# Kernel tuning notes

Hardware: AMD Instinct MI355X
Metric: run time of the kernel (lower is better)

## Reference

```python
import jax, jax.numpy as jnp
import numpy as np

DIM = 768
HQ = 8
HKV = 2
HD = 64
B = 1
S = 4096


def setup_inputs() -> dict:
    key = jax.random.key(0)
    ks = jax.random.split(key, 9)
    s = 0.02
    return {
        "x": jax.random.normal(ks[0], (B, S, DIM), jnp.float32),
        "Wq": jax.random.normal(ks[1], (DIM, HQ * HD), jnp.float32) * s,
        "bq": jax.random.normal(ks[2], (HQ * HD,), jnp.float32) * s,
        "Wk": jax.random.normal(ks[3], (DIM, HKV * HD), jnp.float32) * s,
        "bk": jax.random.normal(ks[4], (HKV * HD,), jnp.float32) * s,
        "Wv": jax.random.normal(ks[5], (DIM, HKV * HD), jnp.float32) * s,
        "bv": jax.random.normal(ks[6], (HKV * HD,), jnp.float32) * s,
        "Wo": jax.random.normal(ks[7], (HQ * HD, DIM), jnp.float32) * s,
        "bo": jax.random.normal(ks[8], (DIM,), jnp.float32) * s,
    }


def reference(x, Wq, bq, Wk, bk, Wv, bv, Wo, bo):
    bsz, q_len, _ = x.shape
    n_rep = HQ // HKV
    # projections
    q = (x @ Wq + bq).reshape(bsz, q_len, HQ, HD).transpose(0, 2, 1, 3)   # [b,hq,s,d]
    k = (x @ Wk + bk).reshape(bsz, q_len, HKV, HD).transpose(0, 2, 1, 3)  # [b,hkv,s,d]
    v = (x @ Wv + bv).reshape(bsz, q_len, HKV, HD).transpose(0, 2, 1, 3)
    # repeat_kv: expand kv heads to match query heads
    k = jnp.broadcast_to(k[:, :, None], (bsz, HKV, n_rep, q_len, HD)).reshape(bsz, HQ, q_len, HD)
    v = jnp.broadcast_to(v[:, :, None], (bsz, HKV, n_rep, q_len, HD)).reshape(bsz, HQ, q_len, HD)
    # full materialized attention (no mask in the original)
    att = jnp.einsum("bhqd,bhkd->bhqk", q, k) / jnp.sqrt(jnp.float32(HD))
    att = jax.nn.softmax(att.astype(jnp.float32), axis=-1).astype(q.dtype)  # [b,hq,s,s]
    out = jnp.einsum("bhqk,bhkd->bhqd", att, v)
    out = out.transpose(0, 2, 1, 3).reshape(bsz, q_len, HQ * HD)
    out = out @ Wo + bo
    return (out, att)
```

## Files before the change

kernel.cpp:

```cpp
#include <hip/hip_runtime.h>
#include <hip/hip_bf16.h>


#define DIM   768
#define Sc    4096

typedef __bf16 bfrag __attribute__((ext_vector_type(8)));
typedef float  facc  __attribute__((ext_vector_type(4)));

#define MFMA_BF16(a,b,c) __builtin_amdgcn_mfma_f32_16x16x32_bf16((a),(b),(c),0,0,0)

__global__ __launch_bounds__(256) void prep_kernel(
    const float* __restrict__ x,  const float* __restrict__ Wq,
    const float* __restrict__ Wk, const float* __restrict__ Wv,
    const float* __restrict__ Wo,
    __bf16* __restrict__ xb, __bf16* __restrict__ WqkvT, __bf16* __restrict__ WobT)
{
  int i = blockIdx.x * 256 + threadIdx.x;
  const int NX = Sc * DIM;
  const int NW = DIM * DIM;
  if (i < NX) { xb[i] = (__bf16)x[i]; return; }
  i -= NX;
  if (i < NW) {
    int n = i / DIM, c = i - n * DIM;
    float v;
    if (n < 512)      v = Wq[c * 512 + n];
    else if (n < 640) v = Wk[c * 128 + (n - 512)];
    else              v = Wv[c * 128 + (n - 640)];
    WqkvT[i] = (__bf16)v;
    return;
  }
  i -= NW;
  {
    int n = i / 512, k = i - n * 512;
    WobT[i] = (__bf16)Wo[k * DIM + n];
  }
}

template<int MODE>
__global__ __launch_bounds__(256) void gemm_kernel(
    const __bf16* __restrict__ A, const __bf16* __restrict__ BT, int Kd,
    const float* __restrict__ b0, const float* __restrict__ b1, const float* __restrict__ b2,
    __bf16* __restrict__ Qb, __bf16* __restrict__ Kb, __bf16* __restrict__ VTb,
    float* __restrict__ Cout)
{
  const int tid  = threadIdx.x;
  const int w    = tid >> 6;
  const int lane = tid & 63;
  const int i16  = lane & 15;
  const int quad = lane >> 4;
  const int n0   = blockIdx.x * 64;
  const int m0   = blockIdx.y * 128;

  __shared__ __attribute__((aligned(16))) __bf16 Al[128 * 72];
  __shared__ __attribute__((aligned(16))) __bf16 Bl[64 * 72];

  facc acc[2][4];
#pragma unroll
  for (int mt = 0; mt < 2; ++mt)
#pragma unroll
    for (int nt = 0; nt < 4; ++nt)
      acc[mt][nt] = (facc){0.f, 0.f, 0.f, 0.f};

  const int nkt = Kd >> 6;
  for (int kt = 0; kt < nkt; ++kt) {
#pragma unroll
    for (int it = 0; it < 4; ++it) {
      int idx = tid + it * 256;
      int r = idx >> 3, ch = idx & 7;
      *(uint4*)&Al[r * 72 + ch * 8] =
          *(const uint4*)(A + (size_t)(m0 + r) * Kd + (kt * 64 + ch * 8));
    }
#pragma unroll
    for (int it = 0; it < 2; ++it) {
      int idx = tid + it * 256;
      int r = idx >> 3, ch = idx & 7;
      *(uint4*)&Bl[r * 72 + ch * 8] =
          *(const uint4*)(BT + (size_t)(n0 + r) * Kd + (kt * 64 + ch * 8));
    }
    __syncthreads();
#pragma unroll
    for (int ks = 0; ks < 2; ++ks) {
      bfrag a0 = *(const bfrag*)&Al[(w * 32 + i16) * 72 + ks * 32 + quad * 8];
      bfrag a1 = *(const bfrag*)&Al[(w * 32 + 16 + i16) * 72 + ks * 32 + quad * 8];
#pragma unroll
      for (int nt = 0; nt < 4; ++nt) {
        bfrag b = *(const bfrag*)&Bl[(nt * 16 + i16) * 72 + ks * 32 + quad * 8];
        acc[0][nt] = MFMA_BF16(a0, b, acc[0][nt]);
        acc[1][nt] = MFMA_BF16(a1, b, acc[1][nt]);
      }
    }
    __syncthreads();
  }

#pragma unroll
  for (int mt = 0; mt < 2; ++mt)
#pragma unroll
    for (int nt = 0; nt < 4; ++nt) {
      const int n = n0 + nt * 16 + i16;
      const int rbase = m0 + w * 32 + mt * 16 + quad * 4;
      if (MODE == 0) {
        float bias;
        if (n < 512)      bias = b0[n];
        else if (n < 640) bias = b1[n - 512];
        else              bias = b2[n - 640];
#pragma unroll
        for (int reg = 0; reg < 4; ++reg) {
          float v = acc[mt][nt][reg] + bias;
          int row = rbase + reg;
          if (n < 512) {
            int hh = n >> 6, d = n & 63;
            Qb[((size_t)hh * Sc + row) * 64 + d] = (__bf16)(v * 0.125f);
          } else if (n < 640) {
            int hh = (n - 512) >> 6, d = n & 63;
            Kb[((size_t)hh * Sc + row) * 64 + d] = (__bf16)v;
          } else {
            int hh = (n - 640) >> 6, d = n & 63;
            VTb[(size_t)hh * 64 * Sc + (size_t)d * Sc + row] = (__bf16)v;
          }
        }
      } else {
        float bias = b0[n];
#pragma unroll
        for (int reg = 0; reg < 4; ++reg)
          Cout[(size_t)(rbase + reg) * DIM + n] = acc[mt][nt][reg] + bias;
      }
    }
}

__global__ __launch_bounds__(256) void attn_kernel(
    const __bf16* __restrict__ Qb, const __bf16* __restrict__ Kb,
    const __bf16* __restrict__ VTb,
    float* __restrict__ att, __bf16* __restrict__ OAb)
{
  const int tid  = threadIdx.x;
  const int w    = tid >> 6;
  const int lane = tid & 63;
  const int i16  = lane & 15;
  const int quad = lane >> 4;
  const int h    = blockIdx.y;
  const int kvh  = h >> 2;
  const int q0   = blockIdx.x * 128;

  __shared__ __attribute__((aligned(16))) __bf16 Kl[64 * 72];
  __shared__ __attribute__((aligned(16))) __bf16 Vl[64 * 72];
  __shared__ __attribute__((aligned(16))) __bf16 Pl[128 * 72];

  bfrag qf[2][2];
#pragma unroll
  for (int mt = 0; mt < 2; ++mt)
#pragma unroll
    for (int ks = 0; ks < 2; ++ks)
      qf[mt][ks] = *(const bfrag*)(Qb +
          ((size_t)h * Sc + q0 + w * 32 + mt * 16 + i16) * 64 + ks * 32 + quad * 8);

  float mrun[2][4], lrun[2][4];
#pragma unroll
  for (int mt = 0; mt < 2; ++mt)
#pragma unroll
    for (int r = 0; r < 4; ++r) { mrun[mt][r] = -1e30f; lrun[mt][r] = 0.f; }

  const __bf16* Kbase = Kb  + (size_t)kvh * Sc * 64;
  const __bf16* Vbase = VTb + (size_t)kvh * 64 * Sc;

  for (int kt = 0; kt < 64; ++kt) {
#pragma unroll
    for (int it = 0; it < 2; ++it) {
      int idx = tid + it * 256; int r = idx >> 3, ch = idx & 7;
      *(uint4*)&Kl[r * 72 + ch * 8] =
          *(const uint4*)(Kbase + (size_t)(kt * 64 + r) * 64 + ch * 8);
    }
    __syncthreads();
    facc s[2][4];
#pragma unroll
    for (int mt = 0; mt < 2; ++mt)
#pragma unroll
      for (int nt = 0; nt < 4; ++nt)
        s[mt][nt] = (facc){0.f, 0.f, 0.f, 0.f};
#pragma unroll
    for (int ks = 0; ks < 2; ++ks)
#pragma unroll
      for (int mt = 0; mt < 2; ++mt) {
        bfrag a = qf[mt][ks];
#pragma unroll
        for (int nt = 0; nt < 4; ++nt) {
          bfrag b = *(const bfrag*)&Kl[(nt * 16 + i16) * 72 + ks * 32 + quad * 8];
          s[mt][nt] = MFMA_BF16(a, b, s[mt][nt]);
        }
      }
#pragma unroll
    for (int mt = 0; mt < 2; ++mt)
#pragma unroll
      for (int r = 0; r < 4; ++r) {
        float tm = fmaxf(fmaxf(s[mt][0][r], s[mt][1][r]), fmaxf(s[mt][2][r], s[mt][3][r]));
        tm = fmaxf(tm, __shfl_xor(tm, 1));
        tm = fmaxf(tm, __shfl_xor(tm, 2));
        tm = fmaxf(tm, __shfl_xor(tm, 4));
        tm = fmaxf(tm, __shfl_xor(tm, 8));
        float mnew = fmaxf(mrun[mt][r], tm);
        float ts = __expf(s[mt][0][r] - mnew) + __expf(s[mt][1][r] - mnew)
                 + __expf(s[mt][2][r] - mnew) + __expf(s[mt][3][r] - mnew);
        ts += __shfl_xor(ts, 1);
        ts += __shfl_xor(ts, 2);
        ts += __shfl_xor(ts, 4);
        ts += __shfl_xor(ts, 8);
        lrun[mt][r] = lrun[mt][r] * __expf(mrun[mt][r] - mnew) + ts;
        mrun[mt][r] = mnew;
      }
    __syncthreads();
  }

  float linv[2][4];
#pragma unroll
  for (int mt = 0; mt < 2; ++mt)
#pragma unroll
    for (int r = 0; r < 4; ++r) linv[mt][r] = 1.f / lrun[mt][r];

  facc oacc[2][4];
#pragma unroll
  for (int mt = 0; mt < 2; ++mt)
#pragma unroll
    for (int nt = 0; nt < 4; ++nt)
      oacc[mt][nt] = (facc){0.f, 0.f, 0.f, 0.f};

  float* attb = att + (size_t)h * Sc * Sc;

  for (int kt = 0; kt < 64; ++kt) {
#pragma unroll
    for (int it = 0; it < 2; ++it) {
      int idx = tid + it * 256; int r = idx >> 3, ch = idx & 7;
      *(uint4*)&Kl[r * 72 + ch * 8] =
          *(const uint4*)(Kbase + (size_t)(kt * 64 + r) * 64 + ch * 8);
    }
#pragma unroll
    for (int it = 0; it < 2; ++it) {
      int idx = tid + it * 256; int r = idx >> 3, ch = idx & 7;
      *(uint4*)&Vl[r * 72 + ch * 8] =
          *(const uint4*)(Vbase + (size_t)r * Sc + kt * 64 + ch * 8);
    }
    __syncthreads();
    facc s[2][4];
#pragma unroll
    for (int mt = 0; mt < 2; ++mt)
#pragma unroll
      for (int nt = 0; nt < 4; ++nt)
        s[mt][nt] = (facc){0.f, 0.f, 0.f, 0.f};
#pragma unroll
    for (int ks = 0; ks < 2; ++ks)
#pragma unroll
      for (int mt = 0; mt < 2; ++mt) {
        bfrag a = qf[mt][ks];
#pragma unroll
        for (int nt = 0; nt < 4; ++nt) {
          bfrag b = *(const bfrag*)&Kl[(nt * 16 + i16) * 72 + ks * 32 + quad * 8];
          s[mt][nt] = MFMA_BF16(a, b, s[mt][nt]);
        }
      }
#pragma unroll
    for (int mt = 0; mt < 2; ++mt)
#pragma unroll
      for (int nt = 0; nt < 4; ++nt)
#pragma unroll
        for (int r = 0; r < 4; ++r) {
          float p = __expf(s[mt][nt][r] - mrun[mt][r]) * linv[mt][r];
          int row = q0 + w * 32 + mt * 16 + quad * 4 + r;
          attb[(size_t)row * Sc + kt * 64 + nt * 16 + i16] = p;
          Pl[(w * 32 + mt * 16 + quad * 4 + r) * 72 + nt * 16 + i16] = (__bf16)p;
        }
#pragma unroll
    for (int ks = 0; ks < 2; ++ks)
#pragma unroll
      for (int mt = 0; mt < 2; ++mt) {
        bfrag pa = *(const bfrag*)&Pl[(w * 32 + mt * 16 + i16) * 72 + ks * 32 + quad * 8];
#pragma unroll
        for (int nt = 0; nt < 4; ++nt) {
          bfrag bvv = *(const bfrag*)&Vl[(nt * 16 + i16) * 72 + ks * 32 + quad * 8];
          oacc[mt][nt] = MFMA_BF16(pa, bvv, oacc[mt][nt]);
        }
      }
    __syncthreads();
  }

#pragma unroll
  for (int mt = 0; mt < 2; ++mt)
#pragma unroll
    for (int nt = 0; nt < 4; ++nt)
#pragma unroll
      for (int r = 0; r < 4; ++r) {
        int row = q0 + w * 32 + mt * 16 + quad * 4 + r;
        OAb[(size_t)row * 512 + h * 64 + nt * 16 + i16] = (__bf16)oacc[mt][nt][r];
      }
}

extern "C" void kernel_launch(void* const* d_in, const int* in_sizes, int n_in,
                              void* d_out, int out_size, void* d_ws, size_t ws_size,
                              hipStream_t stream) {
  const float* x  = (const float*)d_in[0];
  const float* Wq = (const float*)d_in[1];
  const float* bq = (const float*)d_in[2];
  const float* Wk = (const float*)d_in[3];
  const float* bk = (const float*)d_in[4];
  const float* Wv = (const float*)d_in[5];
  const float* bv = (const float*)d_in[6];
  const float* Wo = (const float*)d_in[7];
  const float* bo = (const float*)d_in[8];

  float* out = (float*)d_out;
  float* att = out + (size_t)Sc * DIM;

  char* ws = (char*)d_ws;
  size_t off = 0;
  __bf16* xb    = (__bf16*)(ws + off); off += (size_t)Sc * DIM * 2;
  __bf16* WqkvT = (__bf16*)(ws + off); off += (size_t)DIM * DIM * 2;
  __bf16* WobT  = (__bf16*)(ws + off); off += (size_t)DIM * 512 * 2;
  __bf16* Qb    = (__bf16*)(ws + off); off += (size_t)8 * Sc * 64 * 2;
  __bf16* Kb    = (__bf16*)(ws + off); off += (size_t)2 * Sc * 64 * 2;
  __bf16* VTb   = (__bf16*)(ws + off); off += (size_t)2 * 64 * Sc * 2;
  __bf16* OAb   = (__bf16*)(ws + off); off += (size_t)Sc * 512 * 2;

  prep_kernel<<<16128, 256, 0, stream>>>(x, Wq, Wk, Wv, Wo, xb, WqkvT, WobT);
  gemm_kernel<0><<<dim3(12, 32), 256, 0, stream>>>(xb, WqkvT, 768, bq, bk, bv,
                                                   Qb, Kb, VTb, nullptr);
  attn_kernel<<<dim3(32, 8), 256, 0, stream>>>(Qb, Kb, VTb, att, OAb);
  gemm_kernel<1><<<dim3(12, 32), 256, 0, stream>>>(OAb, WobT, 512, bo, nullptr, nullptr,
                                                   nullptr, nullptr, nullptr, out);
}
```

Measured before the change: 929.2 us.

## Split attention keys across waves with 16-query blocks and coalesced att stores

The attention kernel now processes 16 query rows per block and splits the 4096 keys across the four waves. Each wave keeps its own softmax statistics, and these are merged through shared memory before the second pass. Probabilities are staged in LDS so the large fp32 attention matrix is written with coalesced 16-byte stores, and K/V are read directly from global memory rather than through shared tiles. The GEMMs use 64-row tiles with twice as many blocks, trading per-block reuse for more parallelism. The attention grid grows to 2048 blocks with a launch-bounds occupancy hint, at the cost of more redundant K/V loads from L2.

```diff
diff --git a/kernel.cpp b/kernel.cpp
--- a/kernel.cpp
+++ b/kernel.cpp
@@ -50,22 +50,19 @@
   const int i16  = lane & 15;
   const int quad = lane >> 4;
   const int n0   = blockIdx.x * 64;
-  const int m0   = blockIdx.y * 128;
-
-  __shared__ __attribute__((aligned(16))) __bf16 Al[128 * 72];
+  const int m0   = blockIdx.y * 64;
+
+  __shared__ __attribute__((aligned(16))) __bf16 Al[64 * 72];
   __shared__ __attribute__((aligned(16))) __bf16 Bl[64 * 72];
 
-  facc acc[2][4];
-#pragma unroll
-  for (int mt = 0; mt < 2; ++mt)
-#pragma unroll
-    for (int nt = 0; nt < 4; ++nt)
-      acc[mt][nt] = (facc){0.f, 0.f, 0.f, 0.f};
+  facc acc[4];
+#pragma unroll
+  for (int nt = 0; nt < 4; ++nt) acc[nt] = (facc){0.f, 0.f, 0.f, 0.f};
 
   const int nkt = Kd >> 6;
   for (int kt = 0; kt < nkt; ++kt) {
 #pragma unroll
-    for (int it = 0; it < 4; ++it) {
+    for (int it = 0; it < 2; ++it) {
       int idx = tid + it * 256;
       int r = idx >> 3, ch = idx & 7;
       *(uint4*)&Al[r * 72 + ch * 8] =
@@ -81,54 +78,53 @@
     __syncthreads();
 #pragma unroll
     for (int ks = 0; ks < 2; ++ks) {
-      bfrag a0 = *(const bfrag*)&Al[(w * 32 + i16) * 72 + ks * 32 + quad * 8];
-      bfrag a1 = *(const bfrag*)&Al[(w * 32 + 16 + i16) * 72 + ks * 32 + quad * 8];
+      bfrag a = *(const bfrag*)&Al[(w * 16 + i16) * 72 + ks * 32 + quad * 8];
 #pragma unroll
       for (int nt = 0; nt < 4; ++nt) {
         bfrag b = *(const bfrag*)&Bl[(nt * 16 + i16) * 72 + ks * 32 + quad * 8];
-        acc[0][nt] = MFMA_BF16(a0, b, acc[0][nt]);
-        acc[1][nt] = MFMA_BF16(a1, b, acc[1][nt]);
+        acc[nt] = MFMA_BF16(a, b, acc[nt]);
       }
     }
     __syncthreads();
   }
 
 #pragma unroll
-  for (int mt = 0; mt < 2; ++mt)
-#pragma unroll
-    for (int nt = 0; nt < 4; ++nt) {
-      const int n = n0 + nt * 16 + i16;
-      const int rbase = m0 + w * 32 + mt * 16 + quad * 4;
-      if (MODE == 0) {
-        float bias;
-        if (n < 512)      bias = b0[n];
-        else if (n < 640) bias = b1[n - 512];
-        else              bias = b2[n - 640];
-#pragma unroll
-        for (int reg = 0; reg < 4; ++reg) {
-          float v = acc[mt][nt][reg] + bias;
-          int row = rbase + reg;
-          if (n < 512) {
-            int hh = n >> 6, d = n & 63;
-            Qb[((size_t)hh * Sc + row) * 64 + d] = (__bf16)(v * 0.125f);
-          } else if (n < 640) {
-            int hh = (n - 512) >> 6, d = n & 63;
-            Kb[((size_t)hh * Sc + row) * 64 + d] = (__bf16)v;
-          } else {
-            int hh = (n - 640) >> 6, d = n & 63;
-            VTb[(size_t)hh * 64 * Sc + (size_t)d * Sc + row] = (__bf16)v;
-          }
+  for (int nt = 0; nt < 4; ++nt) {
+    const int n = n0 + nt * 16 + i16;
+    const int rbase = m0 + w * 16 + quad * 4;
+    if (MODE == 0) {
+      float bias;
+      if (n < 512)      bias = b0[n];
+      else if (n < 640) bias = b1[n - 512];
+      else              bias = b2[n - 640];
+#pragma unroll
+      for (int reg = 0; reg < 4; ++reg) {
+        float v = acc[nt][reg] + bias;
+        int row = rbase + reg;
+        if (n < 512) {
+          int hh = n >> 6, d = n & 63;
+          Qb[((size_t)hh * Sc + row) * 64 + d] = (__bf16)(v * 0.125f);
+        } else if (n < 640) {
+          int hh = (n - 512) >> 6, d = n & 63;
+          Kb[((size_t)hh * Sc + row) * 64 + d] = (__bf16)v;
+        } else {
+          int hh = (n - 640) >> 6, d = n & 63;
+          VTb[(size_t)hh * 64 * Sc + (size_t)d * Sc + row] = (__bf16)v;
         }
-      } else {
-        float bias = b0[n];
-#pragma unroll
-        for (int reg = 0; reg < 4; ++reg)
-          Cout[(size_t)(rbase + reg) * DIM + n] = acc[mt][nt][reg] + bias;
-      }
-    }
+      }
+    } else {
+      float bias = b0[n];
+#pragma unroll
+      for (int reg = 0; reg < 4; ++reg)
+        Cout[(size_t)(rbase + reg) * DIM + n] = acc[nt][reg] + bias;
+    }
+  }
 }
 
-__global__ __launch_bounds__(256) void attn_kernel(
+#define PFSTRIDE 68
+#define PFWAVE   (16 * PFSTRIDE + 4)
+
+__global__ __launch_bounds__(256, 6) void attn_kernel(
     const __bf16* __restrict__ Qb, const __bf16* __restrict__ Kb,
     const __bf16* __restrict__ VTb,
     float* __restrict__ att, __bf16* __restrict__ OAb)
@@ -140,156 +136,138 @@
   const int quad = lane >> 4;
   const int h    = blockIdx.y;
   const int kvh  = h >> 2;
-  const int q0   = blockIdx.x * 128;
-
-  __shared__ __attribute__((aligned(16))) __bf16 Kl[64 * 72];
-  __shared__ __attribute__((aligned(16))) __bf16 Vl[64 * 72];
-  __shared__ __attribute__((aligned(16))) __bf16 Pl[128 * 72];
-
-  bfrag qf[2][2];
-#pragma unroll
-  for (int mt = 0; mt < 2; ++mt)
-#pragma unroll
-    for (int ks = 0; ks < 2; ++ks)
-      qf[mt][ks] = *(const bfrag*)(Qb +
-          ((size_t)h * Sc + q0 + w * 32 + mt * 16 + i16) * 64 + ks * 32 + quad * 8);
-
-  float mrun[2][4], lrun[2][4];
-#pragma unroll
-  for (int mt = 0; mt < 2; ++mt)
-#pragma unroll
-    for (int r = 0; r < 4; ++r) { mrun[mt][r] = -1e30f; lrun[mt][r] = 0.f; }
+  const int q0   = blockIdx.x * 16;
+
+  __shared__ __attribute__((aligned(16))) float Pf[4 * PFWAVE];
+  __shared__ float SM[4][16], SL[4][16];
 
   const __bf16* Kbase = Kb  + (size_t)kvh * Sc * 64;
   const __bf16* Vbase = VTb + (size_t)kvh * 64 * Sc;
 
-  for (int kt = 0; kt < 64; ++kt) {
-#pragma unroll
-    for (int it = 0; it < 2; ++it) {
-      int idx = tid + it * 256; int r = idx >> 3, ch = idx & 7;
-      *(uint4*)&Kl[r * 72 + ch * 8] =
-          *(const uint4*)(Kbase + (size_t)(kt * 64 + r) * 64 + ch * 8);
-    }
-    __syncthreads();
-    facc s[2][4];
-#pragma unroll
-    for (int mt = 0; mt < 2; ++mt)
-#pragma unroll
-      for (int nt = 0; nt < 4; ++nt)
-        s[mt][nt] = (facc){0.f, 0.f, 0.f, 0.f};
+  bfrag qf[2];
+#pragma unroll
+  for (int ks = 0; ks < 2; ++ks)
+    qf[ks] = *(const bfrag*)(Qb + ((size_t)h * Sc + q0 + i16) * 64 + ks * 32 + quad * 8);
+
+  float mrun[4], lrun[4];
+#pragma unroll
+  for (int r = 0; r < 4; ++r) { mrun[r] = -1e30f; lrun[r] = 0.f; }
+
+  const int key0 = w * 1024;
+
+  for (int kt = 0; kt < 16; ++kt) {
+    const int kb0 = key0 + kt * 64;
+    facc s[4];
+#pragma unroll
+    for (int nt = 0; nt < 4; ++nt) s[nt] = (facc){0.f, 0.f, 0.f, 0.f};
 #pragma unroll
     for (int ks = 0; ks < 2; ++ks)
 #pragma unroll
-      for (int mt = 0; mt < 2; ++mt) {
-        bfrag a = qf[mt][ks];
-#pragma unroll
-        for (int nt = 0; nt < 4; ++nt) {
-          bfrag b = *(const bfrag*)&Kl[(nt * 16 + i16) * 72 + ks * 32 + quad * 8];
-          s[mt][nt] = MFMA_BF16(a, b, s[mt][nt]);
-        }
-      }
-#pragma unroll
-    for (int mt = 0; mt < 2; ++mt)
-#pragma unroll
-      for (int r = 0; r < 4; ++r) {
-        float tm = fmaxf(fmaxf(s[mt][0][r], s[mt][1][r]), fmaxf(s[mt][2][r], s[mt][3][r]));
-        tm = fmaxf(tm, __shfl_xor(tm, 1));
-        tm = fmaxf(tm, __shfl_xor(tm, 2));
-        tm = fmaxf(tm, __shfl_xor(tm, 4));
-        tm = fmaxf(tm, __shfl_xor(tm, 8));
-        float mnew = fmaxf(mrun[mt][r], tm);
-        float ts = __expf(s[mt][0][r] - mnew) + __expf(s[mt][1][r] - mnew)
-                 + __expf(s[mt][2][r] - mnew) + __expf(s[mt][3][r] - mnew);
-        ts += __shfl_xor(ts, 1);
-        ts += __shfl_xor(ts, 2);
-        ts += __shfl_xor(ts, 4);
-        ts += __shfl_xor(ts, 8);
-        lrun[mt][r] = lrun[mt][r] * __expf(mrun[mt][r] - mnew) + ts;
-        mrun[mt][r] = mnew;
-      }
-    __syncthreads();
-  }
-
-  float linv[2][4];
-#pragma unroll
-  for (int mt = 0; mt < 2; ++mt)
-#pragma unroll
-    for (int r = 0; r < 4; ++r) linv[mt][r] = 1.f / lrun[mt][r];
-
-  facc oacc[2][4];
-#pragma unroll
-  for (int mt = 0; mt < 2; ++mt)
+      for (int nt = 0; nt < 4; ++nt) {
+        bfrag kf = *(const bfrag*)(Kbase + (size_t)(kb0 + nt * 16 + i16) * 64 + ks * 32 + quad * 8);
+        s[nt] = MFMA_BF16(qf[ks], kf, s[nt]);
+      }
+#pragma unroll
+    for (int r = 0; r < 4; ++r) {
+      float tm = fmaxf(fmaxf(s[0][r], s[1][r]), fmaxf(s[2][r], s[3][r]));
+      tm = fmaxf(tm, __shfl_xor(tm, 1));
+      tm = fmaxf(tm, __shfl_xor(tm, 2));
+      tm = fmaxf(tm, __shfl_xor(tm, 4));
+      tm = fmaxf(tm, __shfl_xor(tm, 8));
+      float mnew = fmaxf(mrun[r], tm);
+      float ts = __expf(s[0][r] - mnew) + __expf(s[1][r] - mnew)
+               + __expf(s[2][r] - mnew) + __expf(s[3][r] - mnew);
+      ts += __shfl_xor(ts, 1);
+      ts += __shfl_xor(ts, 2);
+      ts += __shfl_xor(ts, 4);
+      ts += __shfl_xor(ts, 8);
+      lrun[r] = lrun[r] * __expf(mrun[r] - mnew) + ts;
+      mrun[r] = mnew;
+    }
+  }
+
+  if (i16 == 0) {
+#pragma unroll
+    for (int r = 0; r < 4; ++r) { SM[w][quad * 4 + r] = mrun[r]; SL[w][quad * 4 + r] = lrun[r]; }
+  }
+  __syncthreads();
+  float mglob[4], linv[4];
+#pragma unroll
+  for (int r = 0; r < 4; ++r) {
+    const int rr = quad * 4 + r;
+    float m0v = SM[0][rr], m1v = SM[1][rr], m2v = SM[2][rr], m3v = SM[3][rr];
+    float mg = fmaxf(fmaxf(m0v, m1v), fmaxf(m2v, m3v));
+    float lg = SL[0][rr] * __expf(m0v - mg) + SL[1][rr] * __expf(m1v - mg)
+             + SL[2][rr] * __expf(m2v - mg) + SL[3][rr] * __expf(m3v - mg);
+    mglob[r] = mg;
+    linv[r]  = 1.f / lg;
+  }
+
+  facc oacc[4];
+#pragma unroll
+  for (int nt = 0; nt < 4; ++nt) oacc[nt] = (facc){0.f, 0.f, 0.f, 0.f};
+
+  float* attb = att + (size_t)h * Sc * Sc;
+  float* Pw   = Pf + w * PFWAVE;
+
+  for (int kt = 0; kt < 16; ++kt) {
+    const int kb0 = key0 + kt * 64;
+    facc s[4];
+#pragma unroll
+    for (int nt = 0; nt < 4; ++nt) s[nt] = (facc){0.f, 0.f, 0.f, 0.f};
+#pragma unroll
+    for (int ks = 0; ks < 2; ++ks)
+#pragma unroll
+      for (int nt = 0; nt < 4; ++nt) {
+        bfrag kf = *(const bfrag*)(Kbase + (size_t)(kb0 + nt * 16 + i16) * 64 + ks * 32 + quad * 8);
+        s[nt] = MFMA_BF16(qf[ks], kf, s[nt]);
+      }
 #pragma unroll
     for (int nt = 0; nt < 4; ++nt)
-      oacc[mt][nt] = (facc){0.f, 0.f, 0.f, 0.f};
-
-  float* attb = att + (size_t)h * Sc * Sc;
-
-  for (int kt = 0; kt < 64; ++kt) {
-#pragma unroll
-    for (int it = 0; it < 2; ++it) {
-      int idx = tid + it * 256; int r = idx >> 3, ch = idx & 7;
-      *(uint4*)&Kl[r * 72 + ch * 8] =
-          *(const uint4*)(Kbase + (size_t)(kt * 64 + r) * 64 + ch * 8);
-    }
-#pragma unroll
-    for (int it = 0; it < 2; ++it) {
-      int idx = tid + it * 256; int r = idx >> 3, ch = idx & 7;
-      *(uint4*)&Vl[r * 72 + ch * 8] =
-          *(const uint4*)(Vbase + (size_t)r * Sc + kt * 64 + ch * 8);
-    }
-    __syncthreads();
-    facc s[2][4];
-#pragma unroll
-    for (int mt = 0; mt < 2; ++mt)
-#pragma unroll
-      for (int nt = 0; nt < 4; ++nt)
-        s[mt][nt] = (facc){0.f, 0.f, 0.f, 0.f};
+#pragma unroll
+      for (int r = 0; r < 4; ++r)
+        Pw[(quad * 4 + r) * PFSTRIDE + nt * 16 + i16] =
+            __expf(s[nt][r] - mglob[r]) * linv[r];
+    bfrag pa[2];
+#pragma unroll
+    for (int ks = 0; ks < 2; ++ks) {
+      facc p0 = *(const facc*)&Pw[i16 * PFSTRIDE + ks * 32 + quad * 8];
+      facc p1 = *(const facc*)&Pw[i16 * PFSTRIDE + ks * 32 + quad * 8 + 4];
+      bfrag t;
+      t[0] = (__bf16)p0[0]; t[1] = (__bf16)p0[1]; t[2] = (__bf16)p0[2]; t[3] = (__bf16)p0[3];
+      t[4] = (__bf16)p1[0]; t[5] = (__bf16)p1[1]; t[6] = (__bf16)p1[2]; t[7] = (__bf16)p1[3];
+      pa[ks] = t;
+    }
 #pragma unroll
     for (int ks = 0; ks < 2; ++ks)
 #pragma unroll
-      for (int mt = 0; mt < 2; ++mt) {
-        bfrag a = qf[mt][ks];
-#pragma unroll
-        for (int nt = 0; nt < 4; ++nt) {
-          bfrag b = *(const bfrag*)&Kl[(nt * 16 + i16) * 72 + ks * 32 + quad * 8];
-          s[mt][nt] = MFMA_BF16(a, b, s[mt][nt]);
-        }
-      }
-#pragma unroll
-    for (int mt = 0; mt < 2; ++mt)
-#pragma unroll
-      for (int nt = 0; nt < 4; ++nt)
-#pragma unroll
-        for (int r = 0; r < 4; ++r) {
-          float p = __expf(s[mt][nt][r] - mrun[mt][r]) * linv[mt][r];
-          int row = q0 + w * 32 + mt * 16 + quad * 4 + r;
-          attb[(size_t)row * Sc + kt * 64 + nt * 16 + i16] = p;
-          Pl[(w * 32 + mt * 16 + quad * 4 + r) * 72 + nt * 16 + i16] = (__bf16)p;
-        }
-#pragma unroll
-    for (int ks = 0; ks < 2; ++ks)
-#pragma unroll
-      for (int mt = 0; mt < 2; ++mt) {
-        bfrag pa = *(const bfrag*)&Pl[(w * 32 + mt * 16 + i16) * 72 + ks * 32 + quad * 8];
-#pragma unroll
-        for (int nt = 0; nt < 4; ++nt) {
-          bfrag bvv = *(const bfrag*)&Vl[(nt * 16 + i16) * 72 + ks * 32 + quad * 8];
-          oacc[mt][nt] = MFMA_BF16(pa, bvv, oacc[mt][nt]);
-        }
-      }
-    __syncthreads();
-  }
-
-#pragma unroll
-  for (int mt = 0; mt < 2; ++mt)
-#pragma unroll
-    for (int nt = 0; nt < 4; ++nt)
-#pragma unroll
-      for (int r = 0; r < 4; ++r) {
-        int row = q0 + w * 32 + mt * 16 + quad * 4 + r;
-        OAb[(size_t)row * 512 + h * 64 + nt * 16 + i16] = (__bf16)oacc[mt][nt][r];
-      }
+      for (int nt = 0; nt < 4; ++nt) {
+        bfrag vf = *(const bfrag*)(Vbase + (size_t)(nt * 16 + i16) * Sc + kb0 + ks * 32 + quad * 8);
+        oacc[nt] = MFMA_BF16(pa[ks], vf, oacc[nt]);
+      }
+#pragma unroll
+    for (int it = 0; it < 4; ++it) {
+      int flat = it * 64 + lane;
+      int row = flat >> 4, c4 = flat & 15;
+      facc v = *(const facc*)&Pw[row * PFSTRIDE + c4 * 4];
+      *(facc*)&attb[(size_t)(q0 + row) * Sc + kb0 + c4 * 4] = v;
+    }
+  }
+
+#pragma unroll
+  for (int nt = 0; nt < 4; ++nt)
+#pragma unroll
+    for (int r = 0; r < 4; ++r)
+      Pw[(quad * 4 + r) * PFSTRIDE + nt * 16 + i16] = oacc[nt][r];
+  __syncthreads();
+#pragma unroll
+  for (int it = 0; it < 4; ++it) {
+    int e = it * 256 + tid;
+    int row = e >> 6, d = e & 63;
+    float sum = Pf[0 * PFWAVE + row * PFSTRIDE + d] + Pf[1 * PFWAVE + row * PFSTRIDE + d]
+              + Pf[2 * PFWAVE + row * PFSTRIDE + d] + Pf[3 * PFWAVE + row * PFSTRIDE + d];
+    OAb[(size_t)(q0 + row) * 512 + h * 64 + d] = (__bf16)sum;
+  }
 }
 
 extern "C" void kernel_launch(void* const* d_in, const int* in_sizes, int n_in,
@@ -319,9 +297,9 @@
   __bf16* OAb   = (__bf16*)(ws + off); off += (size_t)Sc * 512 * 2;
 
   prep_kernel<<<16128, 256, 0, stream>>>(x, Wq, Wk, Wv, Wo, xb, WqkvT, WobT);
-  gemm_kernel<0><<<dim3(12, 32), 256, 0, stream>>>(xb, WqkvT, 768, bq, bk, bv,
+  gemm_kernel<0><<<dim3(12, 64), 256, 0, stream>>>(xb, WqkvT, 768, bq, bk, bv,
                                                    Qb, Kb, VTb, nullptr);
-  attn_kernel<<<dim3(32, 8), 256, 0, stream>>>(Qb, Kb, VTb, att, OAb);
-  gemm_kernel<1><<<dim3(12, 32), 256, 0, stream>>>(OAb, WobT, 512, bo, nullptr, nullptr,
+  attn_kernel<<<dim3(256, 8), 256, 0, stream>>>(Qb, Kb, VTb, att, OAb);
+  gemm_kernel<1><<<dim3(12, 64), 256, 0, stream>>>(OAb, WobT, 512, bo, nullptr, nullptr,
                                                    nullptr, nullptr, nullptr, out);
 }
```

After: 877.1 us. 1.06x faster.
